# Kernel tuning notes

Measured on AMD Instinct MI355X. Metric: run time of the kernel, lower is better.

Reference implementation:

```python
import jax, jax.numpy as jnp
import numpy as np

WS = 7          # window size (fixed: last_idx=169=(2*7-1)^2)
NP = 1          # num_priorset
NH = 8          # num heads
DIM = 256
SHIFT = 3
N = WS * WS     # 49 tokens per window
NK = N + 3 * NP # 52 K/V tokens (window + uk/fg/bg priors)


def _rel_index():
    coords = np.stack(np.meshgrid(np.arange(WS), np.arange(WS), indexing='ij')).reshape(2, -1)
    rel = (coords[:, :, None] - coords[:, None, :]).transpose(1, 2, 0).astype(np.int64)
    rel[:, :, 0] += WS - 1
    rel[:, :, 1] += WS - 1
    rel[:, :, 0] *= 2 * WS - 1
    idx = rel.sum(-1)                      # (49,49) in [0,168]
    full = np.full((N, NK), 169, dtype=np.int64)
    full[:, :N] = idx
    for j in range(3 * NP):
        full[:, N + j] = 169 + j           # dedicated bias rows for priors
    return jnp.asarray(full)

REL_IDX = _rel_index()


def _ln(t, g, b, eps=1e-5):
    mu = t.mean(-1, keepdims=True)
    var = ((t - mu) ** 2).mean(-1, keepdims=True)
    return (t - mu) * jax.lax.rsqrt(var + eps) * g + b


def setup_inputs() -> dict:
    key = jax.random.key(0)
    ks = jax.random.split(key, 16)
    B, H, W, C = 4, 112, 112, DIM
    nW = (H // WS) * (W // WS)
    hid = 4 * C
    inp = {
        'x': jax.random.normal(ks[0], (B, H * W, C), jnp.float32),
        'mask_matrix': jax.random.normal(ks[1], (nW, N, N), jnp.float32),
        'area_fg': jax.random.uniform(ks[2], (B, H, W, 1), jnp.float32),
        'area_bg': jax.random.uniform(ks[3], (B, H, W, 1), jnp.float32),
        'area_uk': jax.random.uniform(ks[4], (B, H, W, 1), jnp.float32),
        'norm1_g': jnp.ones((C,), jnp.float32),
        'norm1_b': jnp.zeros((C,), jnp.float32),
        'norm2_g': jnp.ones((C,), jnp.float32),
        'norm2_b': jnp.zeros((C,), jnp.float32),
        'qkv_w': jax.random.normal(ks[5], (3 * C, C), jnp.float32) * 0.02,
        'qkv_b': jnp.zeros((3 * C,), jnp.float32),
        'proj_w': jax.random.normal(ks[6], (C, C), jnp.float32) * 0.02,
        'proj_b': jnp.zeros((C,), jnp.float32),
        'rel_table': jax.random.normal(ks[7], (169 + 3 * NP, NH), jnp.float32) * 0.02,
        'fc1_w': jax.random.normal(ks[8], (hid, C), jnp.float32) * 0.02,
        'fc1_b': jnp.zeros((hid,), jnp.float32),
        'fc2_w': jax.random.normal(ks[9], (C, hid), jnp.float32) * 0.02,
        'fc2_b': jnp.zeros((C,), jnp.float32),
        'H': 112,
        'W': 112,
    }
    return inp


def reference(x, mask_matrix, area_fg, area_bg, area_uk,
              norm1_g, norm1_b, norm2_g, norm2_b,
              qkv_w, qkv_b, proj_w, proj_b, rel_table,
              fc1_w, fc1_b, fc2_w, fc2_b, H, W):
    B, L, C = x.shape
    d = C // NH
    scale = d ** -0.5
    nWh, nWw = H // WS, W // WS
    nW = nWh * nWw

    shortcut = x
    x4 = x.reshape(B, H, W, C)
    eps = 1e-9
    # masked global-average prior tokens (B, C)
    def pooled(area):
        return (area * x4).sum((1, 2)) / (area.sum((1, 2)) + eps)
    uk, fg, bg = pooled(area_uk), pooled(area_fg), pooled(area_bg)

    xn = _ln(x, norm1_g, norm1_b).reshape(B, H, W, C)
    uk_n = _ln(uk, norm1_g, norm1_b)
    fg_n = _ln(fg, norm1_g, norm1_b)
    bg_n = _ln(bg, norm1_g, norm1_b)

    # cyclic shift + window partition (H,W divisible by WS -> no padding)
    xs = jnp.roll(xn, (-SHIFT, -SHIFT), (1, 2))
    xw = xs.reshape(B, nWh, WS, nWw, WS, C).transpose(0, 1, 3, 2, 4, 5).reshape(B * nW, N, C)

    # prior highway tokens (order: unknown, fg, bg) and per-window copies
    ph = jnp.stack([uk_n, fg_n, bg_n], axis=1)                      # (B,3,C)
    pr = jnp.broadcast_to(ph[:, None], (B, nW, 3, C)).reshape(B * nW, 3, C)
    xk = jnp.concatenate([xw, pr], axis=1)                          # (B_,52,C)

    qkv = (xk @ qkv_w.T + qkv_b).reshape(B * nW, NK, 3, NH, d)
    q = qkv[:, :N, 0].transpose(0, 2, 1, 3) * scale                 # (B_,h,49,d)
    k = qkv[:, :, 1].transpose(0, 2, 1, 3)                          # (B_,h,52,d)
    v = qkv[:, :, 2].transpose(0, 2, 1, 3)

    attn = jnp.einsum('bhnd,bhmd->bhnm', q, k)                      # (B_,h,49,52)
    bias = rel_table[REL_IDX].transpose(2, 0, 1)                    # (h,49,52)
    attn = attn + bias[None]
    mask = jnp.pad(mask_matrix, ((0, 0), (0, 0), (0, 3 * NP)))      # (nW,49,52)
    attn = attn.reshape(B, nW, NH, N, NK) + mask[None, :, None]
    attn = jax.nn.softmax(attn.reshape(B * nW, NH, N, NK), axis=-1)

    out = jnp.einsum('bhnm,bhmd->bhnd', attn, v)
    out = out.transpose(0, 2, 1, 3).reshape(B * nW, N, C)
    out = out @ proj_w.T + proj_b

    # prior highway: qkv on priors, keep V, project
    ph_qkv = (ph @ qkv_w.T + qkv_b).reshape(B, 3 * NP, 3, NH, d)
    v_hw = ph_qkv[:, :, 2].reshape(B, 3 * NP, C) @ proj_w.T + proj_b

    # window reverse + reverse shift
    xo = out.reshape(B, nWh, nWw, WS, WS, C).transpose(0, 1, 3, 2, 4, 5).reshape(B, H, W, C)
    xo = jnp.roll(xo, (SHIFT, SHIFT), (1, 2)).reshape(B, L, C)

    x = shortcut + xo
    h = _ln(x, norm2_g, norm2_b)
    h = jax.nn.gelu(h @ fc1_w.T + fc1_b, approximate=False)
    x = x + (h @ fc2_w.T + fc2_b)
    return x, v_hw
```

## Files before the change

kernel.cpp:

```cpp
#include <hip/hip_runtime.h>
#include <hip/hip_bf16.h>
#include <math.h>

typedef __bf16 bf16;
typedef bf16 bf16x8 __attribute__((ext_vector_type(8)));
typedef bf16 bf16x4 __attribute__((ext_vector_type(4)));
typedef float f32x4 __attribute__((ext_vector_type(4)));

constexpr int DIM   = 256;
constexpr int NH    = 8;
constexpr int LTOT  = 112 * 112;
constexpr int BTOT  = 4;
constexpr int MROWS = BTOT * LTOT;
constexpr int MQKV  = MROWS + BTOT * 3;
constexpr int NTOK  = 49;
constexpr int NKV   = 52;

__global__ __launch_bounds__(256) void cvt_all(
    const float* __restrict__ qkvw, const float* __restrict__ projw,
    const float* __restrict__ fc1w, const float* __restrict__ fc2w,
    bf16* __restrict__ d)
{
    int i = blockIdx.x * 256 + threadIdx.x;
    float v;
    if (i < 196608)      v = qkvw[i];
    else if (i < 262144) v = projw[i - 196608];
    else if (i < 524288) v = fc1w[i - 262144];
    else                 v = fc2w[i - 524288];
    d[i] = (bf16)v;
}

__global__ __launch_bounds__(256) void pool_partial(
    const float* __restrict__ x, const float* __restrict__ afg,
    const float* __restrict__ abg, const float* __restrict__ auk,
    float* __restrict__ pnum, float* __restrict__ pden)
{
    int b = blockIdx.x / 196, ch = blockIdx.x % 196;
    int p0 = ch * 64, tid = threadIdx.x;
    __shared__ float su[64], sf[64], sb[64];
    if (tid < 64) {
        int p = p0 + tid;
        su[tid] = auk[b * LTOT + p];
        sf[tid] = afg[b * LTOT + p];
        sb[tid] = abg[b * LTOT + p];
    }
    __syncthreads();
    float nu = 0.f, nf = 0.f, nb = 0.f;
    const float* xp = x + ((size_t)b * LTOT + p0) * DIM + tid;
    for (int pp = 0; pp < 64; ++pp) {
        float xv = xp[(size_t)pp * DIM];
        nu += su[pp] * xv; nf += sf[pp] * xv; nb += sb[pp] * xv;
    }
    size_t base = (size_t)blockIdx.x * 3 * DIM + tid;
    pnum[base]           = nu;
    pnum[base + DIM]     = nf;
    pnum[base + 2 * DIM] = nb;
    if (tid < 3) {
        const float* sptr = tid == 0 ? su : (tid == 1 ? sf : sb);
        float t = 0.f;
        for (int i = 0; i < 64; ++i) t += sptr[i];
        pden[blockIdx.x * 3 + tid] = t;
    }
}

__device__ __forceinline__ void block_meanvar(float v, float& mu, float& rstd, float eps) {
    float s = v, s2 = v * v;
    #pragma unroll
    for (int o = 32; o >= 1; o >>= 1) { s += __shfl_down(s, o); s2 += __shfl_down(s2, o); }
    __shared__ float ps[4], ps2[4];
    int w = threadIdx.x >> 6, ln = threadIdx.x & 63;
    if (ln == 0) { ps[w] = s; ps2[w] = s2; }
    __syncthreads();
    float S  = ps[0] + ps[1] + ps[2] + ps[3];
    float S2 = ps2[0] + ps2[1] + ps2[2] + ps2[3];
    mu = S * (1.f / 256.f);
    float var = S2 * (1.f / 256.f) - mu * mu;
    rstd = rsqrtf(var + eps);
}

__global__ __launch_bounds__(256) void prior_ln(
    const float* __restrict__ pnum, const float* __restrict__ pden,
    const float* __restrict__ g, const float* __restrict__ bt, bf16* __restrict__ xn)
{
    int b = blockIdx.x / 3, j = blockIdx.x % 3, tid = threadIdx.x;
    float s = 0.f, den = 0.f;
    for (int ch = 0; ch < 196; ++ch) {
        s   += pnum[((size_t)(b * 196 + ch) * 3 + j) * DIM + tid];
        den += pden[(b * 196 + ch) * 3 + j];
    }
    float v = s / (den + 1e-9f);
    float mu, rs;
    block_meanvar(v, mu, rs, 1e-5f);
    xn[((size_t)MROWS + blockIdx.x) * DIM + tid] = (bf16)((v - mu) * rs * g[tid] + bt[tid]);
}

__global__ __launch_bounds__(512) void ln1_kernel(
    const float* __restrict__ x, const float* __restrict__ g,
    const float* __restrict__ bt, bf16* __restrict__ xn)
{
    const size_t row = (size_t)blockIdx.x * 8 + (threadIdx.x >> 6);
    const int lane = threadIdx.x & 63;
    f32x4 v = *(const f32x4*)(x + row * DIM + lane * 4);
    float s  = v[0] + v[1] + v[2] + v[3];
    float s2 = v[0]*v[0] + v[1]*v[1] + v[2]*v[2] + v[3]*v[3];
    #pragma unroll
    for (int o = 32; o >= 1; o >>= 1) { s += __shfl_xor(s, o); s2 += __shfl_xor(s2, o); }
    float mu = s * (1.f / 256.f);
    float var = s2 * (1.f / 256.f) - mu * mu;
    float rs = rsqrtf(var + 1e-5f);
    f32x4 gv = *(const f32x4*)(g + lane * 4);
    f32x4 bv = *(const f32x4*)(bt + lane * 4);
    bf16x4 o;
    #pragma unroll
    for (int u = 0; u < 4; ++u) o[u] = (bf16)((v[u] - mu) * rs * gv[u] + bv[u]);
    *(bf16x4*)(xn + row * DIM + lane * 4) = o;
}

__device__ __forceinline__ void load_lds16(const void* g, void* l) {
    __builtin_amdgcn_global_load_lds((const __attribute__((address_space(1))) void*)g,
                                     (__attribute__((address_space(3))) void*)l, 16, 0, 0);
}

template <int EPI, int K, int N>
__global__ __launch_bounds__(256) void gemm_bt(
    const bf16* __restrict__ A, const bf16* __restrict__ W,
    const float* __restrict__ bias, bf16* __restrict__ Cb,
    float* __restrict__ Cf, const float* __restrict__ resid, int M)
{
    __shared__ __align__(16) char smem[49152];
    const int tid = threadIdx.x;
    const int wv = tid >> 6, lane = tid & 63;

    const int gx = gridDim.x;
    const int nwg = gx * (int)gridDim.y;
    int lin = blockIdx.y * gx + blockIdx.x;
    int xcd = lin & 7, loc = lin >> 3;
    int qq = nwg >> 3, rr = nwg & 7;
    int nid = (xcd < rr ? xcd * (qq + 1) : rr * (qq + 1) + (xcd - rr) * qq) + loc;
    int by = nid / gx, bx = nid - by * gx;
    const int m0 = by * 128, n0 = bx * 128;

    const int r  = tid >> 2;
    const int kb = (((tid & 3) ^ ((tid >> 3) & 3)) * 8);
    const int wr = (wv >> 1) * 64, wc = (wv & 1) * 64;
    const int fr = lane & 15;
    const int fo = (((lane >> 4) ^ ((fr >> 1) & 3)) * 8);

    int ra0 = m0 + r;      if (ra0 >= M) ra0 = M - 1;
    int ra1 = m0 + r + 64; if (ra1 >= M) ra1 = M - 1;
    const bf16* pA0 = A + (size_t)ra0 * K + kb;
    const bf16* pA1 = A + (size_t)ra1 * K + kb;
    const bf16* pW0 = W + (size_t)(n0 + r) * K + kb;
    const bf16* pW1 = W + (size_t)(n0 + r + 64) * K + kb;

    const f32x4 zero = {0.f, 0.f, 0.f, 0.f};
    f32x4 acc[4][4];
    #pragma unroll
    for (int i = 0; i < 4; ++i)
        #pragma unroll
        for (int j = 0; j < 4; ++j) acc[i][j] = zero;

    constexpr int nK = K >> 5;

    auto stage = [&](int kt, int b) {
        bf16* Ab = (bf16*)(smem + b * 16384);
        bf16* Bb = (bf16*)(smem + b * 16384 + 8192);
        const int off = kt * 32;
        load_lds16(pA0 + off, Ab + wv * 512);
        load_lds16(pA1 + off, Ab + 2048 + wv * 512);
        load_lds16(pW0 + off, Bb + wv * 512);
        load_lds16(pW1 + off, Bb + 2048 + wv * 512);
    };

    stage(0, 0);
    stage(1, 1);

    #pragma unroll
    for (int kt = 0; kt < nK; ++kt) {
        const int cur = kt % 3;
        asm volatile("s_waitcnt lgkmcnt(0)" ::: "memory");
        if (kt < nK - 1) asm volatile("s_waitcnt vmcnt(4)" ::: "memory");
        else             asm volatile("s_waitcnt vmcnt(0)" ::: "memory");
        __builtin_amdgcn_s_barrier();
        if (kt + 2 < nK) stage(kt + 2, (kt + 2) % 3);
        const bf16* Ac = (const bf16*)(smem + cur * 16384);
        const bf16* Bc = (const bf16*)(smem + cur * 16384 + 8192);
        bf16x8 af[4], bw[4];
        #pragma unroll
        for (int i = 0; i < 4; ++i) af[i] = *(const bf16x8*)(Ac + (wr + i * 16 + fr) * 32 + fo);
        #pragma unroll
        for (int i = 0; i < 4; ++i) bw[i] = *(const bf16x8*)(Bc + (wc + i * 16 + fr) * 32 + fo);
        #pragma unroll
        for (int i = 0; i < 4; ++i)
            #pragma unroll
            for (int j = 0; j < 4; ++j)
                acc[i][j] = __builtin_amdgcn_mfma_f32_16x16x32_bf16(af[i], bw[j], acc[i][j], 0, 0, 0);
    }
    __syncthreads();

    const int cr = (lane >> 4) * 4, cc = lane & 15;
    if constexpr (EPI == 3) {
        float* Cs = (float*)smem;
        #pragma unroll
        for (int half = 0; half < 2; ++half) {
            if (wr == half * 64) {
                #pragma unroll
                for (int i = 0; i < 4; ++i)
                    #pragma unroll
                    for (int j = 0; j < 4; ++j) {
                        const int col = wc + j * 16 + cc;
                        const float bv = bias[n0 + col];
                        #pragma unroll
                        for (int q = 0; q < 4; ++q)
                            Cs[(i * 16 + cr + q) * 132 + col] = acc[i][j][q] + bv;
                    }
            }
            __syncthreads();
            for (int p = tid; p < 2048; p += 256) {
                const int row = p >> 5, seg = (p & 31) * 4;
                const int gr = m0 + half * 64 + row;
                if (gr < M) {
                    f32x4 v = *(const f32x4*)(Cs + row * 132 + seg);
                    const size_t o = (size_t)gr * N + n0 + seg;
                    f32x4 rv = *(const f32x4*)(resid + o);
                    *(f32x4*)(Cf + o) = v + rv;
                }
            }
            __syncthreads();
        }
    } else {
        bf16* Csb = (bf16*)smem;
        #pragma unroll
        for (int i = 0; i < 4; ++i)
            #pragma unroll
            for (int j = 0; j < 4; ++j) {
                const int col = wc + j * 16 + cc;
                const float bv = bias[n0 + col];
                #pragma unroll
                for (int q = 0; q < 4; ++q) {
                    float v = acc[i][j][q] + bv;
                    if constexpr (EPI == 2) {
                        float u = 0.7978845608028654f * (v + 0.044715f * v * v * v);
                        v = v / (1.f + __expf(-2.f * u));
                    }
                    Csb[(wr + i * 16 + cr + q) * 144 + col] = (bf16)v;
                }
            }
        __syncthreads();
        for (int p = tid; p < 2048; p += 256) {
            const int row = p >> 4, seg = (p & 15) * 8;
            const int gr = m0 + row;
            if (gr < M)
                *(bf16x8*)(Cb + (size_t)gr * N + n0 + seg) = *(const bf16x8*)(Csb + row * 144 + seg);
        }
    }
}

__global__ __launch_bounds__(256) void proj_ln2(
    const bf16* __restrict__ A, const bf16* __restrict__ W,
    const float* __restrict__ bias, const float* __restrict__ x,
    const float* __restrict__ g, const float* __restrict__ bt,
    float* __restrict__ x2, bf16* __restrict__ ln2)
{
    __shared__ __align__(16) char smem[40960];
    bf16* As = (bf16*)smem;
    bf16* Bs = (bf16*)(smem + 8192);

    const int tid = threadIdx.x;
    const int wv = tid >> 6, lane = tid & 63;
    const int m0 = blockIdx.x * 64;

    const int r4 = tid >> 2;
    const int kb = (((tid & 3) ^ ((tid >> 3) & 3)) * 8);
    const int fr = lane & 15;
    const int fo = (((lane >> 4) ^ ((fr >> 1) & 3)) * 8);

    const bf16* pA  = A + (size_t)(m0 + r4) * 256 + kb;
    const bf16* pW0 = W + (size_t)(r4)       * 256 + kb;
    const bf16* pW1 = W + (size_t)(r4 + 64)  * 256 + kb;
    const bf16* pW2 = W + (size_t)(r4 + 128) * 256 + kb;
    const bf16* pW3 = W + (size_t)(r4 + 192) * 256 + kb;

    const f32x4 zero = {0.f, 0.f, 0.f, 0.f};
    f32x4 acc[4][4];
    #pragma unroll
    for (int i = 0; i < 4; ++i)
        #pragma unroll
        for (int j = 0; j < 4; ++j) acc[i][j] = zero;

    auto stage = [&](int kt, int b) {
        const int off = kt * 32;
        load_lds16(pA  + off, As + b * 2048 + wv * 512);
        load_lds16(pW0 + off, Bs + b * 8192 + wv * 512);
        load_lds16(pW1 + off, Bs + b * 8192 + 2048 + wv * 512);
        load_lds16(pW2 + off, Bs + b * 8192 + 4096 + wv * 512);
        load_lds16(pW3 + off, Bs + b * 8192 + 6144 + wv * 512);
    };

    stage(0, 0);
    __syncthreads();
    #pragma unroll
    for (int kt = 0; kt < 8; ++kt) {
        const int cur = kt & 1;
        if (kt + 1 < 8) stage(kt + 1, cur ^ 1);
        const bf16* Ac = As + cur * 2048;
        const bf16* Bc = Bs + cur * 8192;
        bf16x8 af[4], bw[4];
        #pragma unroll
        for (int i = 0; i < 4; ++i) af[i] = *(const bf16x8*)(Ac + (i * 16 + fr) * 32 + fo);
        #pragma unroll
        for (int j = 0; j < 4; ++j) bw[j] = *(const bf16x8*)(Bc + (wv * 64 + j * 16 + fr) * 32 + fo);
        #pragma unroll
        for (int i = 0; i < 4; ++i)
            #pragma unroll
            for (int j = 0; j < 4; ++j)
                acc[i][j] = __builtin_amdgcn_mfma_f32_16x16x32_bf16(af[i], bw[j], acc[i][j], 0, 0, 0);
        __syncthreads();
    }

    float* Cs = (float*)smem;
    const int cr = (lane >> 4) * 4, cc = lane & 15;
    const f32x4 gv  = *(const f32x4*)(g  + lane * 4);
    const f32x4 bv2 = *(const f32x4*)(bt + lane * 4);
    #pragma unroll
    for (int h = 0; h < 2; ++h) {
        #pragma unroll
        for (int i2 = 0; i2 < 2; ++i2) {
            const int i = h * 2 + i2;
            #pragma unroll
            for (int j = 0; j < 4; ++j) {
                const int col = wv * 64 + j * 16 + cc;
                const float bv = bias[col];
                #pragma unroll
                for (int q = 0; q < 4; ++q)
                    Cs[(i2 * 16 + cr + q) * 260 + col] = acc[i][j][q] + bv;
            }
        }
        __syncthreads();
        #pragma unroll
        for (int it = 0; it < 8; ++it) {
            const int rl = wv * 8 + it;
            const int ar = m0 + h * 32 + rl;
            int bwin = ar / 49;
            int n = ar - bwin * 49;
            int bb = bwin >> 8, w = bwin & 255;
            int ni = n / 7, nj = n - ni * 7;
            int hh = (w >> 4) * 7 + ni + 3;  if (hh >= 112) hh -= 112;
            int ww2 = (w & 15) * 7 + nj + 3; if (ww2 >= 112) ww2 -= 112;
            const size_t nrow = (size_t)(bb * LTOT + hh * 112 + ww2);
            f32x4 pv = *(const f32x4*)(Cs + rl * 260 + lane * 4);
            f32x4 xv = *(const f32x4*)(x + nrow * 256 + lane * 4);
            f32x4 v = pv + xv;
            float s1 = v[0] + v[1] + v[2] + v[3];
            float s2 = v[0]*v[0] + v[1]*v[1] + v[2]*v[2] + v[3]*v[3];
            #pragma unroll
            for (int o = 32; o >= 1; o >>= 1) { s1 += __shfl_xor(s1, o); s2 += __shfl_xor(s2, o); }
            float mu = s1 * (1.f / 256.f);
            float rs = rsqrtf(s2 * (1.f / 256.f) - mu * mu + 1e-5f);
            *(f32x4*)(x2 + nrow * 256 + lane * 4) = v;
            bf16x4 ov;
            #pragma unroll
            for (int u = 0; u < 4; ++u) ov[u] = (bf16)((v[u] - mu) * rs * gv[u] + bv2[u]);
            *(bf16x4*)(ln2 + nrow * 256 + lane * 4) = ov;
        }
        __syncthreads();
    }
}

__global__ __launch_bounds__(512, 1) void attn_kernel(
    const bf16* __restrict__ qkv, const float* __restrict__ mask,
    const float* __restrict__ rel, bf16* __restrict__ att_out)
{
    __shared__ int rowtab[52];
    __shared__ float mLds[64 * 67];
    __shared__ float rLds[1376];
    __shared__ __align__(16) bf16 vT[8 * 32 * 80];
    __shared__ __align__(16) bf16 pbuf[8 * 64 * 80];

    const int tid = threadIdx.x;
    const int bw = blockIdx.x;
    const int b = bw >> 8, w = bw & 255;
    const int wh = w >> 4, wwi = w & 15;

    if (tid < 52) {
        int row;
        if (tid < 49) {
            int i = tid / 7, j = tid % 7;
            int gh = wh * 7 + i + 3;  if (gh >= 112) gh -= 112;
            int gw = wwi * 7 + j + 3; if (gw >= 112) gw -= 112;
            row = b * LTOT + gh * 112 + gw;
        } else {
            row = MROWS + b * 3 + (tid - 49);
        }
        rowtab[tid] = row;
    }
    __syncthreads();

    for (int e = tid; e < 64 * 67; e += 512) {
        int q = e / 67, k = e % 67;
        mLds[e] = (q < 49 && k < 49) ? mask[(size_t)w * 2401 + q * 49 + k] : 0.f;
    }
    for (int e = tid; e < 1376; e += 512) rLds[e] = rel[e];
    for (int e = tid; e < 256 * 12; e += 512) {
        int rr = e / 12, c = 52 + e % 12;
        vT[rr * 80 + c] = (bf16)0.f;
    }
    for (int e = tid; e < 52 * 256; e += 512) {
        int key = e >> 8, c = e & 255;
        vT[c * 80 + key] = qkv[(size_t)rowtab[key] * 768 + 512 + c];
    }
    __syncthreads();

    const int h    = tid >> 6;
    const int lane = tid & 63;
    const int cl   = lane & 15;
    const int hi4  = lane >> 4;
    const int cr   = hi4 * 4;
    const int fo   = hi4 * 8;

    bf16x8 kf[4], qf[4];
    #pragma unroll
    for (int i = 0; i < 4; ++i) {
        int key = 16 * i + cl; if (key > 51) key = 51;
        kf[i] = *(const bf16x8*)(qkv + (size_t)rowtab[key] * 768 + 256 + h * 32 + fo);
    }
    #pragma unroll
    for (int j = 0; j < 4; ++j) {
        int qq = 16 * j + cl; if (qq > 48) qq = 48;
        qf[j] = *(const bf16x8*)(qkv + (size_t)rowtab[qq] * 768 + h * 32 + fo);
    }
    const f32x4 zero = {0.f, 0.f, 0.f, 0.f};
    f32x4 acc[4][4];
    #pragma unroll
    for (int i = 0; i < 4; ++i)
        #pragma unroll
        for (int j = 0; j < 4; ++j) acc[i][j] = zero;
    __builtin_amdgcn_s_setprio(1);
    #pragma unroll
    for (int i = 0; i < 4; ++i)
        #pragma unroll
        for (int j = 0; j < 4; ++j)
            acc[i][j] = __builtin_amdgcn_mfma_f32_16x16x32_bf16(kf[i], qf[j], acc[i][j], 0, 0, 0);
    __builtin_amdgcn_s_setprio(0);

    int kb[4][4];
    #pragma unroll
    for (int i = 0; i < 4; ++i)
        #pragma unroll
        for (int r = 0; r < 4; ++r) {
            int key = 16 * i + cr + r;
            kb[i][r] = (key / 7) * 13 + (key % 7);
        }
    bf16* pW = pbuf + h * (64 * 80);
    #pragma unroll
    for (int j = 0; j < 4; ++j) {
        const int q = 16 * j + cl;
        const int i1 = q / 7, j1 = q % 7;
        const int qb = (i1 + 6) * 13 + (j1 + 6);
        float sv[16];
        float mx = -3e38f;
        #pragma unroll
        for (int i = 0; i < 4; ++i)
            #pragma unroll
            for (int r = 0; r < 4; ++r) {
                int key = 16 * i + cr + r;
                int idx = key < 49 ? (qb - kb[i][r]) : (169 + key - 49);
                idx = idx < 0 ? 0 : (idx > 171 ? 171 : idx);
                float s = acc[i][j][r] * 0.17677669529663687f
                        + mLds[q * 67 + key] + rLds[idx * 8 + h];
                if (key >= 52) s = -3e38f;
                sv[i * 4 + r] = s;
                mx = fmaxf(mx, s);
            }
        mx = fmaxf(mx, __shfl_xor(mx, 16));
        mx = fmaxf(mx, __shfl_xor(mx, 32));
        float sum = 0.f;
        #pragma unroll
        for (int e = 0; e < 16; ++e) { float p = __expf(sv[e] - mx); sv[e] = p; sum += p; }
        sum += __shfl_xor(sum, 16);
        sum += __shfl_xor(sum, 32);
        const float inv = 1.f / sum;
        #pragma unroll
        for (int i = 0; i < 4; ++i) {
            bf16x4 pk;
            #pragma unroll
            for (int r = 0; r < 4; ++r) pk[r] = (bf16)(sv[i * 4 + r] * inv);
            *(bf16x4*)(pW + q * 80 + 16 * i + cr) = pk;
        }
    }

    f32x4 oacc[4][2];
    #pragma unroll
    for (int i = 0; i < 4; ++i) { oacc[i][0] = zero; oacc[i][1] = zero; }
    #pragma unroll
    for (int ks = 0; ks < 2; ++ks) {
        bf16x8 vf[2];
        #pragma unroll
        for (int j2 = 0; j2 < 2; ++j2)
            vf[j2] = *(const bf16x8*)(vT + (h * 32 + 16 * j2 + cl) * 80 + 32 * ks + fo);
        __builtin_amdgcn_s_setprio(1);
        #pragma unroll
        for (int i = 0; i < 4; ++i) {
            bf16x8 pf = *(const bf16x8*)(pW + (16 * i + cl) * 80 + 32 * ks + fo);
            #pragma unroll
            for (int j2 = 0; j2 < 2; ++j2)
                oacc[i][j2] = __builtin_amdgcn_mfma_f32_16x16x32_bf16(pf, vf[j2], oacc[i][j2], 0, 0, 0);
        }
        __builtin_amdgcn_s_setprio(0);
    }

    #pragma unroll
    for (int i = 0; i < 4; ++i)
        #pragma unroll
        for (int r = 0; r < 4; ++r) {
            int q = 16 * i + cr + r;
            if (q < 49) {
                bf16* op = att_out + ((size_t)bw * 49 + q) * 256 + h * 32 + cl;
                op[0]  = (bf16)oacc[i][0][r];
                op[16] = (bf16)oacc[i][1][r];
            }
        }
}

__global__ __launch_bounds__(256) void vhw_kernel(
    const bf16* __restrict__ qkv, const float* __restrict__ pw,
    const float* __restrict__ pb, float* __restrict__ outp)
{
    int rowI = blockIdx.x;
    int c = threadIdx.x;
    const bf16* vp = qkv + (size_t)(MROWS + rowI) * 768 + 512;
    const float* wr_ = pw + (size_t)c * DIM;
    float acc = pb[c];
    for (int k = 0; k < DIM; ++k) acc += (float)vp[k] * wr_[k];
    outp[(size_t)rowI * DIM + c] = acc;
}

extern "C" void kernel_launch(void* const* d_in, const int* in_sizes, int n_in,
                              void* d_out, int out_size, void* d_ws, size_t ws_size,
                              hipStream_t stream)
{
    const float* x     = (const float*)d_in[0];
    const float* mask  = (const float*)d_in[1];
    const float* afg   = (const float*)d_in[2];
    const float* abg   = (const float*)d_in[3];
    const float* auk   = (const float*)d_in[4];
    const float* n1g   = (const float*)d_in[5];
    const float* n1b   = (const float*)d_in[6];
    const float* n2g   = (const float*)d_in[7];
    const float* n2b   = (const float*)d_in[8];
    const float* qkvw  = (const float*)d_in[9];
    const float* qkvb  = (const float*)d_in[10];
    const float* projw = (const float*)d_in[11];
    const float* projb = (const float*)d_in[12];
    const float* rel   = (const float*)d_in[13];
    const float* fc1w  = (const float*)d_in[14];
    const float* fc1b  = (const float*)d_in[15];
    const float* fc2w  = (const float*)d_in[16];
    const float* fc2b  = (const float*)d_in[17];
    float* out = (float*)d_out;
    char*  ws  = (char*)d_ws;

    bf16*  wq   = (bf16*)(ws + 0);
    bf16*  wp   = (bf16*)(ws + 393216);
    bf16*  wf1  = (bf16*)(ws + 524288);
    bf16*  wf2  = (bf16*)(ws + 1048576);
    float* pnum = (float*)(ws + (28ull << 20));
    float* pden = (float*)(ws + (28ull << 20) + 2408448);
    bf16* xn    = (bf16*)(ws + (2ull << 20));
    bf16* atto  = (bf16*)(ws + (2ull << 20));
    bf16* hbuf  = (bf16*)(ws + (2ull << 20));
    bf16* qkvo  = (bf16*)(ws + (28ull << 20));
    bf16* ln2b  = (bf16*)(ws + (102ull << 20));

    cvt_all<<<3072, 256, 0, stream>>>(qkvw, projw, fc1w, fc2w, (bf16*)ws);

    pool_partial<<<BTOT * 196, 256, 0, stream>>>(x, afg, abg, auk, pnum, pden);
    prior_ln<<<12, 256, 0, stream>>>(pnum, pden, n1g, n1b, xn);
    ln1_kernel<<<MROWS / 8, 512, 0, stream>>>(x, n1g, n1b, xn);

    gemm_bt<0, 256, 768><<<dim3(6, 393), 256, 0, stream>>>(xn, wq, qkvb, qkvo, nullptr, nullptr, MQKV);

    attn_kernel<<<BTOT * 256, 512, 0, stream>>>(qkvo, mask, rel, atto);
    vhw_kernel<<<12, 256, 0, stream>>>(qkvo, projw, projb, out + (size_t)MROWS * DIM);

    proj_ln2<<<MROWS / 64, 256, 0, stream>>>(atto, wp, projb, x, n2g, n2b, out, ln2b);

    gemm_bt<2, 256, 1024><<<dim3(8, 392), 256, 0, stream>>>(ln2b, wf1, fc1b, hbuf, nullptr, nullptr, MROWS);

    gemm_bt<3, 1024, 256><<<dim3(2, 392), 256, 0, stream>>>(hbuf, wf2, fc2b, nullptr, out, out, MROWS);

    (void)in_sizes; (void)n_in; (void)out_size; (void)ws_size;
}
```

Before: 295.9 us.

## Keep softmax probabilities in registers via lane shuffles instead of LDS buffer

The attention kernel no longer writes normalized probabilities to a shared-memory buffer and reads them back for the PV MFMA. Instead it packs them to bf16 pairs and redistributes them across lanes with shuffles into the MFMA A-operand layout, interleaving the PV matmul with each softmax row block. Removing the large pbuf LDS allocation allows launch bounds of two blocks per CU, raising occupancy. The cost is extra shuffle instructions and more register pressure under the tighter bound.

```diff
diff --git a/kernel.cpp b/kernel.cpp
--- a/kernel.cpp
+++ b/kernel.cpp
@@ -367,7 +367,13 @@
     }
 }
 
-__global__ __launch_bounds__(512, 1) void attn_kernel(
+__device__ __forceinline__ unsigned pk2(float a, float b) {
+    union { bf16 h[2]; unsigned u; } c;
+    c.h[0] = (bf16)a; c.h[1] = (bf16)b;
+    return c.u;
+}
+
+__global__ __launch_bounds__(512, 2) void attn_kernel(
     const bf16* __restrict__ qkv, const float* __restrict__ mask,
     const float* __restrict__ rel, bf16* __restrict__ att_out)
 {
@@ -375,7 +381,6 @@
     __shared__ float mLds[64 * 67];
     __shared__ float rLds[1376];
     __shared__ __align__(16) bf16 vT[8 * 32 * 80];
-    __shared__ __align__(16) bf16 pbuf[8 * 64 * 80];
 
     const int tid = threadIdx.x;
     const int bw = blockIdx.x;
@@ -451,7 +456,11 @@
             int key = 16 * i + cr + r;
             kb[i][r] = (key / 7) * 13 + (key % 7);
         }
-    bf16* pW = pbuf + h * (64 * 80);
+
+    f32x4 oacc[4][2];
+    #pragma unroll
+    for (int i = 0; i < 4; ++i) { oacc[i][0] = zero; oacc[i][1] = zero; }
+
     #pragma unroll
     for (int j = 0; j < 4; ++j) {
         const int q = 16 * j + cl;
@@ -480,33 +489,32 @@
         sum += __shfl_xor(sum, 16);
         sum += __shfl_xor(sum, 32);
         const float inv = 1.f / sum;
+
+        int Dw[4][2];
         #pragma unroll
         for (int i = 0; i < 4; ++i) {
-            bf16x4 pk;
-            #pragma unroll
-            for (int r = 0; r < 4; ++r) pk[r] = (bf16)(sv[i * 4 + r] * inv);
-            *(bf16x4*)(pW + q * 80 + 16 * i + cr) = pk;
-        }
-    }
-
-    f32x4 oacc[4][2];
-    #pragma unroll
-    for (int i = 0; i < 4; ++i) { oacc[i][0] = zero; oacc[i][1] = zero; }
-    #pragma unroll
-    for (int ks = 0; ks < 2; ++ks) {
-        bf16x8 vf[2];
-        #pragma unroll
-        for (int j2 = 0; j2 < 2; ++j2)
-            vf[j2] = *(const bf16x8*)(vT + (h * 32 + 16 * j2 + cl) * 80 + 32 * ks + fo);
-        __builtin_amdgcn_s_setprio(1);
-        #pragma unroll
-        for (int i = 0; i < 4; ++i) {
-            bf16x8 pf = *(const bf16x8*)(pW + (16 * i + cl) * 80 + 32 * ks + fo);
-            #pragma unroll
-            for (int j2 = 0; j2 < 2; ++j2)
-                oacc[i][j2] = __builtin_amdgcn_mfma_f32_16x16x32_bf16(pf, vf[j2], oacc[i][j2], 0, 0, 0);
-        }
-        __builtin_amdgcn_s_setprio(0);
+            Dw[i][0] = pk2(sv[i * 4 + 0] * inv, sv[i * 4 + 1] * inv);
+            Dw[i][1] = pk2(sv[i * 4 + 2] * inv, sv[i * 4 + 3] * inv);
+        }
+        #pragma unroll
+        for (int ks = 0; ks < 2; ++ks) {
+            int paw[4];
+            #pragma unroll
+            for (int m = 0; m < 4; ++m) {
+                const int srcLane = cl + (((hi4 & 1) * 2 + (m >> 1)) << 4);
+                int va = __shfl(Dw[2 * ks][m & 1], srcLane);
+                int vb = __shfl(Dw[2 * ks + 1][m & 1], srcLane);
+                paw[m] = (hi4 & 2) ? vb : va;
+            }
+            union { int w[4]; bf16x8 v; } pf;
+            pf.w[0] = paw[0]; pf.w[1] = paw[1]; pf.w[2] = paw[2]; pf.w[3] = paw[3];
+            bf16x8 vf0 = *(const bf16x8*)(vT + (h * 32 + cl)      * 80 + 32 * ks + fo);
+            bf16x8 vf1 = *(const bf16x8*)(vT + (h * 32 + 16 + cl) * 80 + 32 * ks + fo);
+            __builtin_amdgcn_s_setprio(1);
+            oacc[j][0] = __builtin_amdgcn_mfma_f32_16x16x32_bf16(pf.v, vf0, oacc[j][0], 0, 0, 0);
+            oacc[j][1] = __builtin_amdgcn_mfma_f32_16x16x32_bf16(pf.v, vf1, oacc[j][1], 0, 0, 0);
+            __builtin_amdgcn_s_setprio(0);
+        }
     }
 
     #pragma unroll
```

New measurement: 282.0 us. -4.7%, faster.
